# Kernel tuning notes

Measured on AMD Instinct MI355X. Metric: run time of the kernel, lower is better.

## Reference

```python
import jax, jax.numpy as jnp
import numpy as np
import math

B, S, IN_DIM = 4, 2048, 256
ATT_DIM, NUM_HEADS, TOP_K = 128, 4, 32


def _linear_params(key, out_dim, in_dim):
    kw, kb = jax.random.split(key)
    bound = 1.0 / math.sqrt(in_dim)
    w = jax.random.uniform(kw, (out_dim, in_dim), jnp.float32, -bound, bound)
    b = jax.random.uniform(kb, (out_dim,), jnp.float32, -bound, bound)
    return w, b


def setup_inputs() -> dict:
    key = jax.random.key(0)
    keys = jax.random.split(key, 16)
    x = jax.random.normal(keys[0], (B, S, IN_DIM), jnp.float32)
    tp_w, tp_b = _linear_params(keys[1], ATT_DIM, IN_DIM)
    sp_w, sp_b = _linear_params(keys[2], ATT_DIM, IN_DIM)
    ta_qw, ta_qb = _linear_params(keys[3], ATT_DIM, ATT_DIM)
    ta_kw, ta_kb = _linear_params(keys[4], ATT_DIM, ATT_DIM)
    ta_vw, ta_vb = _linear_params(keys[5], ATT_DIM, ATT_DIM)
    ta_ow, ta_ob = _linear_params(keys[6], ATT_DIM, ATT_DIM)
    sa_qw, sa_qb = _linear_params(keys[7], ATT_DIM, ATT_DIM)
    sa_kw, sa_kb = _linear_params(keys[8], ATT_DIM, ATT_DIM)
    sa_vw, sa_vb = _linear_params(keys[9], ATT_DIM, ATT_DIM)
    sa_ow, sa_ob = _linear_params(keys[10], ATT_DIM, ATT_DIM)
    gate_w, gate_b = _linear_params(keys[11], ATT_DIM, 2 * ATT_DIM)
    fus_w, fus_b = _linear_params(keys[12], ATT_DIM, 2 * ATT_DIM)
    return dict(x=x, tp_w=tp_w, tp_b=tp_b, sp_w=sp_w, sp_b=sp_b,
                ta_qw=ta_qw, ta_qb=ta_qb, ta_kw=ta_kw, ta_kb=ta_kb,
                ta_vw=ta_vw, ta_vb=ta_vb, ta_ow=ta_ow, ta_ob=ta_ob,
                sa_qw=sa_qw, sa_qb=sa_qb, sa_kw=sa_kw, sa_kb=sa_kb,
                sa_vw=sa_vw, sa_vb=sa_vb, sa_ow=sa_ow, sa_ob=sa_ob,
                gate_w=gate_w, gate_b=gate_b, fus_w=fus_w, fus_b=fus_b)


def _lin(x, w, b):
    return x @ w.T + b


def _sparse_topk_attention(x, qw, qb, kw, kb, vw, vb, ow, ob):
    # x: [B, S, E]; dropout is identity in eval mode
    b, s, e = x.shape
    h, d = NUM_HEADS, e // NUM_HEADS
    q = _lin(x, qw, qb).reshape(b, s, h, d).transpose(0, 2, 1, 3)  # [B,H,S,D]
    k = _lin(x, kw, kb).reshape(b, s, h, d).transpose(0, 2, 1, 3)
    v = _lin(x, vw, vb).reshape(b, s, h, d).transpose(0, 2, 1, 3)
    scores = jnp.einsum('bhqd,bhkd->bhqk', q, k) / math.sqrt(d)  # [B,H,S,S]
    kk = min(TOP_K, s)
    top_scores, top_idx = jax.lax.top_k(scores, kk)  # [B,H,S,K]
    soft = jax.nn.softmax(top_scores, axis=-1)
    # scatter softmaxed top-k weights into a zero [B,H,S,S] matrix (faithful to source)
    bi = jnp.arange(b)[:, None, None, None]
    hi = jnp.arange(h)[None, :, None, None]
    si = jnp.arange(s)[None, None, :, None]
    sparse = jnp.zeros_like(scores).at[bi, hi, si, top_idx].set(soft)
    out = jnp.einsum('bhqk,bhkd->bhqd', sparse, v)
    out = out.transpose(0, 2, 1, 3).reshape(b, s, e)
    return _lin(out, ow, ob)


def reference(x, tp_w, tp_b, sp_w, sp_b,
              ta_qw, ta_qb, ta_kw, ta_kb, ta_vw, ta_vb, ta_ow, ta_ob,
              sa_qw, sa_qb, sa_kw, sa_kb, sa_vw, sa_vb, sa_ow, sa_ob,
              gate_w, gate_b, fus_w, fus_b):
    temporal = _lin(x, tp_w, tp_b)
    temporal = _sparse_topk_attention(temporal, ta_qw, ta_qb, ta_kw, ta_kb,
                                      ta_vw, ta_vb, ta_ow, ta_ob)
    semantic = _lin(x, sp_w, sp_b)
    semantic = _sparse_topk_attention(semantic, sa_qw, sa_qb, sa_kw, sa_kb,
                                      sa_vw, sa_vb, sa_ow, sa_ob)
    concat = jnp.concatenate([temporal, semantic], axis=-1)  # [B,S,2A]
    gate = jax.nn.sigmoid(_lin(concat, gate_w, gate_b))
    fused = _lin(concat, fus_w, fus_b) * gate
    return fused
```

## Files before the change

### kernel.cpp

```cpp
#include <hip/hip_runtime.h>
#include <math.h>

#define B_   4
#define S_   2048
#define AD   128
#define NH   4
#define HD   32
#define TK   32
#define SEG  1048576
#define CAP  192

#define OFF_PROJ 0
#define OFF_Q    (1 * SEG)
#define OFF_K    (2 * SEG)
#define OFF_V    (3 * SEG)
#define OFF_ATT  (4 * SEG)
#define OFF_T    (5 * SEG)
#define OFF_SB   (6 * SEG)
#define OFF_CAT  (7 * SEG)

__device__ float g_ws[9 * SEG];
__device__ float g_sc[8 * S_ * S_];

__device__ __forceinline__ unsigned f2key(float s) {
    unsigned u = __float_as_uint(s);
    return (u & 0x80000000u) ? ~u : (u | 0x80000000u);
}
__device__ __forceinline__ float key2f(unsigned k) {
    unsigned u = (k & 0x80000000u) ? (k & 0x7FFFFFFFu) : ~k;
    return __uint_as_float(u);
}

template <int KD>
__global__ __launch_bounds__(256)
void lin_kernel(const float* __restrict__ Xext, int xoff,
                const float* __restrict__ W, const float* __restrict__ Bv,
                int yoff)
{
    const float* X = Xext ? Xext : (const float*)(g_ws + xoff);
    float* Y = g_ws + yoff;
    __shared__ float Xs[32][72];
    __shared__ float Ws[32][72];
    const int bm = blockIdx.x * 64;
    const int bn = blockIdx.y * 64;
    const int t  = threadIdx.x;
    const int tx = t & 15, ty = t >> 4;
    const int sr = t >> 3, sc4 = t & 7;
    float acc[4][4] = {};
    for (int kk = 0; kk < KD; kk += 32) {
        #pragma unroll
        for (int it = 0; it < 2; ++it) {
            int rr = sr + it * 32;
            float4 xa = *(const float4*)(X + (size_t)(bm + rr) * KD + kk + sc4 * 4);
            float4 wa = *(const float4*)(W + (size_t)(bn + rr) * KD + kk + sc4 * 4);
            Xs[sc4*4+0][rr] = xa.x; Xs[sc4*4+1][rr] = xa.y;
            Xs[sc4*4+2][rr] = xa.z; Xs[sc4*4+3][rr] = xa.w;
            Ws[sc4*4+0][rr] = wa.x; Ws[sc4*4+1][rr] = wa.y;
            Ws[sc4*4+2][rr] = wa.z; Ws[sc4*4+3][rr] = wa.w;
        }
        __syncthreads();
        #pragma unroll
        for (int kc = 0; kc < 32; ++kc) {
            float4 a4 = *(const float4*)&Xs[kc][ty * 4];
            float4 b4 = *(const float4*)&Ws[kc][tx * 4];
            float a[4] = {a4.x, a4.y, a4.z, a4.w};
            float bb[4] = {b4.x, b4.y, b4.z, b4.w};
            #pragma unroll
            for (int i = 0; i < 4; ++i)
                #pragma unroll
                for (int j = 0; j < 4; ++j)
                    acc[i][j] = fmaf(a[i], bb[j], acc[i][j]);
        }
        __syncthreads();
    }
    #pragma unroll
    for (int i = 0; i < 4; ++i) {
        int row = bm + ty * 4 + i;
        int col = bn + tx * 4;
        float4 o;
        o.x = acc[i][0] + Bv[col + 0]; o.y = acc[i][1] + Bv[col + 1];
        o.z = acc[i][2] + Bv[col + 2]; o.w = acc[i][3] + Bv[col + 3];
        *(float4*)(Y + (size_t)row * AD + col) = o;
    }
}

template <int KD>
__global__ __launch_bounds__(256)
void lin3_kernel(int xoff,
                 const float* __restrict__ W0, const float* __restrict__ B0, int y0,
                 const float* __restrict__ W1, const float* __restrict__ B1, int y1,
                 const float* __restrict__ W2, const float* __restrict__ B2, int y2)
{
    const int z = blockIdx.z;
    const float* X = (const float*)(g_ws + xoff);
    const float* W = (z == 0) ? W0 : (z == 1) ? W1 : W2;
    const float* Bv = (z == 0) ? B0 : (z == 1) ? B1 : B2;
    float* Y = g_ws + ((z == 0) ? y0 : (z == 1) ? y1 : y2);
    __shared__ float Xs[32][72];
    __shared__ float Ws[32][72];
    const int bm = blockIdx.x * 64;
    const int bn = blockIdx.y * 64;
    const int t  = threadIdx.x;
    const int tx = t & 15, ty = t >> 4;
    const int sr = t >> 3, sc4 = t & 7;
    float acc[4][4] = {};
    for (int kk = 0; kk < KD; kk += 32) {
        #pragma unroll
        for (int it = 0; it < 2; ++it) {
            int rr = sr + it * 32;
            float4 xa = *(const float4*)(X + (size_t)(bm + rr) * KD + kk + sc4 * 4);
            float4 wa = *(const float4*)(W + (size_t)(bn + rr) * KD + kk + sc4 * 4);
            Xs[sc4*4+0][rr] = xa.x; Xs[sc4*4+1][rr] = xa.y;
            Xs[sc4*4+2][rr] = xa.z; Xs[sc4*4+3][rr] = xa.w;
            Ws[sc4*4+0][rr] = wa.x; Ws[sc4*4+1][rr] = wa.y;
            Ws[sc4*4+2][rr] = wa.z; Ws[sc4*4+3][rr] = wa.w;
        }
        __syncthreads();
        #pragma unroll
        for (int kc = 0; kc < 32; ++kc) {
            float4 a4 = *(const float4*)&Xs[kc][ty * 4];
            float4 b4 = *(const float4*)&Ws[kc][tx * 4];
            float a[4] = {a4.x, a4.y, a4.z, a4.w};
            float bb[4] = {b4.x, b4.y, b4.z, b4.w};
            #pragma unroll
            for (int i = 0; i < 4; ++i)
                #pragma unroll
                for (int j = 0; j < 4; ++j)
                    acc[i][j] = fmaf(a[i], bb[j], acc[i][j]);
        }
        __syncthreads();
    }
    #pragma unroll
    for (int i = 0; i < 4; ++i) {
        int row = bm + ty * 4 + i;
        int col = bn + tx * 4;
        float4 o;
        o.x = acc[i][0] + Bv[col + 0]; o.y = acc[i][1] + Bv[col + 1];
        o.z = acc[i][2] + Bv[col + 2]; o.w = acc[i][3] + Bv[col + 3];
        *(float4*)(Y + (size_t)row * AD + col) = o;
    }
}

__global__ __launch_bounds__(256)
void score_kernel(int qoff, int koff, int chunk)
{
    const int zh = blockIdx.z;
    const int hh = chunk * 8 + zh, b = hh >> 2, h = hh & 3;
    const float* Qb = g_ws + qoff + (size_t)b * S_ * AD + h * HD;
    const float* Kb = g_ws + koff + (size_t)b * S_ * AD + h * HD;
    float* Sc = g_sc + (size_t)zh * S_ * S_;
    __shared__ float Qs[32][72];
    __shared__ float Ks[32][72];
    const int t = threadIdx.x, tx = t & 15, ty = t >> 4;
    const int sr = t >> 3, sc4 = t & 7;
    const int q0 = blockIdx.y * 64, k0 = blockIdx.x * 64;
    #pragma unroll
    for (int it = 0; it < 2; ++it) {
        int rr = sr + it * 32;
        float4 qa = *(const float4*)(Qb + (size_t)(q0 + rr) * AD + sc4 * 4);
        float4 ka = *(const float4*)(Kb + (size_t)(k0 + rr) * AD + sc4 * 4);
        Qs[sc4*4+0][rr] = qa.x; Qs[sc4*4+1][rr] = qa.y;
        Qs[sc4*4+2][rr] = qa.z; Qs[sc4*4+3][rr] = qa.w;
        Ks[sc4*4+0][rr] = ka.x; Ks[sc4*4+1][rr] = ka.y;
        Ks[sc4*4+2][rr] = ka.z; Ks[sc4*4+3][rr] = ka.w;
    }
    __syncthreads();
    float acc[4][4] = {};
    #pragma unroll
    for (int kc = 0; kc < 32; ++kc) {
        float4 a4 = *(const float4*)&Qs[kc][ty * 4];
        float4 b4 = *(const float4*)&Ks[kc][tx * 4];
        float a[4] = {a4.x, a4.y, a4.z, a4.w};
        float bb[4] = {b4.x, b4.y, b4.z, b4.w};
        #pragma unroll
        for (int i = 0; i < 4; ++i)
            #pragma unroll
            for (int j = 0; j < 4; ++j)
                acc[i][j] = fmaf(a[i], bb[j], acc[i][j]);
    }
    const float scale = 0.17677669529663688f;
    #pragma unroll
    for (int i = 0; i < 4; ++i) {
        float4 o;
        o.x = acc[i][0] * scale; o.y = acc[i][1] * scale;
        o.z = acc[i][2] * scale; o.w = acc[i][3] * scale;
        *(float4*)(Sc + (size_t)(q0 + ty * 4 + i) * S_ + k0 + tx * 4) = o;
    }
}

__device__ __forceinline__ void select_row(const unsigned (&keys)[32],
                                           unsigned long long* sv,
                                           float* wp, unsigned* jp,
                                           int lane, unsigned thr, float Mf)
{
    int base = 0;
    const unsigned long long lt = (1ull << lane) - 1ull;
    #pragma unroll
    for (int t = 0; t < 32; ++t) {
        bool pred = keys[t] >= thr;
        unsigned long long m = __ballot(pred);
        int slot = base + __popcll(m & lt);
        if (pred && slot < CAP) {
            unsigned jidx = (unsigned)((t >> 2) * 256 + lane * 4 + (t & 3));
            sv[slot] = ((unsigned long long)keys[t] << 32) | (unsigned)(2047 - jidx);
        }
        base += __popcll(m);
    }
    const int S = base;
    asm volatile("s_waitcnt lgkmcnt(0)" ::: "memory");

    if (S <= 64) {
        unsigned long long pi = (lane < S) ? sv[lane] : 0ull;
        int rank = 0;
        for (int jx = 0; jx < S; ++jx)
            rank += (sv[jx] > pi) ? 1 : 0;
        float e = 0.f; unsigned ji = 0;
        if (lane < S && rank < TK) {
            float val = key2f((unsigned)(pi >> 32));
            e = __expf(val - Mf);
            ji = 2047u - (unsigned)(pi & 0xFFFFFFFFull);
        }
        float esum = e;
        #pragma unroll
        for (int off = 1; off < 64; off <<= 1) esum += __shfl_xor(esum, off);
        if (lane < S && rank < TK) { wp[rank] = e / esum; jp[rank] = ji; }
    } else if (S <= CAP) {
        unsigned long long pi[3]; int rk[3]; float ee[3]; unsigned jj[3];
        float esum = 0.f;
        #pragma unroll
        for (int u = 0; u < 3; ++u) {
            int i = lane + u * 64;
            pi[u] = (i < S) ? sv[i] : 0ull;
            rk[u] = 0; ee[u] = 0.f; jj[u] = 0;
        }
        for (int jx = 0; jx < S; ++jx) {
            unsigned long long pj = sv[jx];
            #pragma unroll
            for (int u = 0; u < 3; ++u)
                rk[u] += (pj > pi[u]) ? 1 : 0;
        }
        #pragma unroll
        for (int u = 0; u < 3; ++u) {
            int i = lane + u * 64;
            if (i < S && rk[u] < TK) {
                float val = key2f((unsigned)(pi[u] >> 32));
                ee[u] = __expf(val - Mf);
                jj[u] = 2047u - (unsigned)(pi[u] & 0xFFFFFFFFull);
                esum += ee[u];
            }
        }
        #pragma unroll
        for (int off = 1; off < 64; off <<= 1) esum += __shfl_xor(esum, off);
        #pragma unroll
        for (int u = 0; u < 3; ++u) {
            int i = lane + u * 64;
            if (i < S && rk[u] < TK) { wp[rk[u]] = ee[u] / esum; jp[rk[u]] = jj[u]; }
        }
    } else {
        unsigned consumed = 0u;
        for (int i = 0; i < TK; ++i) {
            unsigned bk = 0u; unsigned gj = 0xFFFFFFFFu;
            #pragma unroll
            for (int t = 0; t < 32; ++t) {
                if (((consumed >> t) & 1u) == 0u) {
                    unsigned kk = keys[t];
                    unsigned j = (unsigned)((t >> 2) * 256 + lane * 4 + (t & 3));
                    if (kk > bk || (kk == bk && j < gj)) { bk = kk; gj = j; }
                }
            }
            #pragma unroll
            for (int off = 1; off < 64; off <<= 1) {
                unsigned ok = (unsigned)__shfl_xor((int)bk, off);
                unsigned oj = (unsigned)__shfl_xor((int)gj, off);
                if (ok > bk || (ok == bk && oj < gj)) { bk = ok; gj = oj; }
            }
            if (((gj >> 2) & 63u) == (unsigned)lane && gj != 0xFFFFFFFFu) {
                int t = ((int)gj >> 8) * 4 + ((int)gj & 3);
                consumed |= (1u << t);
            }
            if (lane == 0) { wp[i] = key2f(bk); jp[i] = gj; }
        }
        asm volatile("s_waitcnt lgkmcnt(0)" ::: "memory");
        float v = (lane < TK) ? wp[lane] : 0.f;
        float e = (lane < TK) ? __expf(v - Mf) : 0.f;
        float esum = e;
        #pragma unroll
        for (int off = 1; off < 64; off <<= 1) esum += __shfl_xor(esum, off);
        if (lane < TK) wp[lane] = e / esum;
    }
    asm volatile("s_waitcnt lgkmcnt(0)" ::: "memory");
}

__global__ __launch_bounds__(256)
void topk_kernel(int voff, int ooff, int chunk)
{
    const float* V = g_ws + voff;
    float* O = g_ws + ooff;

    __shared__ unsigned long long sve[4][2][CAP];
    __shared__ float    wsel[4][2][32];
    __shared__ unsigned jsel[4][2][32];

    const int wid  = threadIdx.x >> 6;
    const int lane = threadIdx.x & 63;
    const int gr   = blockIdx.x * 4 + wid;
    const int row0 = gr * 2;
    const int zh   = row0 >> 11;
    const int q0   = row0 & 2047, q1 = q0 + 1;
    const int hh   = chunk * 8 + zh;
    const int b    = hh >> 2,  h = hh & 3;

    const float* Srow0 = g_sc + (size_t)zh * S_ * S_ + (size_t)q0 * S_;
    const float* Srow1 = Srow0 + S_;
    const float* vbase = V + (size_t)b * S_ * AD + h * HD;

    unsigned keys0[32], keys1[32];
    unsigned lmax0 = 0u, lmax1 = 0u;
    #pragma unroll
    for (int i = 0; i < 8; ++i) {
        float4 s4 = ((const float4*)Srow0)[i * 64 + lane];
        unsigned k0 = f2key(s4.x), k1 = f2key(s4.y);
        unsigned k2 = f2key(s4.z), k3 = f2key(s4.w);
        keys0[i*4+0] = k0; keys0[i*4+1] = k1; keys0[i*4+2] = k2; keys0[i*4+3] = k3;
        unsigned m01 = (k0 > k1) ? k0 : k1, m23 = (k2 > k3) ? k2 : k3;
        unsigned m = (m01 > m23) ? m01 : m23;
        lmax0 = (m > lmax0) ? m : lmax0;
    }
    #pragma unroll
    for (int i = 0; i < 8; ++i) {
        float4 s4 = ((const float4*)Srow1)[i * 64 + lane];
        unsigned k0 = f2key(s4.x), k1 = f2key(s4.y);
        unsigned k2 = f2key(s4.z), k3 = f2key(s4.w);
        keys1[i*4+0] = k0; keys1[i*4+1] = k1; keys1[i*4+2] = k2; keys1[i*4+3] = k3;
        unsigned m01 = (k0 > k1) ? k0 : k1, m23 = (k2 > k3) ? k2 : k3;
        unsigned m = (m01 > m23) ? m01 : m23;
        lmax1 = (m > lmax1) ? m : lmax1;
    }

    unsigned bs0 = lmax0, bs1 = lmax1;
    #pragma unroll
    for (int k = 2; k <= 64; k <<= 1) {
        #pragma unroll
        for (int j = k >> 1; j > 0; j >>= 1) {
            unsigned o0 = (unsigned)__shfl_xor((int)bs0, j);
            unsigned o1 = (unsigned)__shfl_xor((int)bs1, j);
            bool keepmin = (((lane & k) == 0) == ((lane & j) == 0));
            bs0 = keepmin ? (bs0 < o0 ? bs0 : o0) : (bs0 > o0 ? bs0 : o0);
            bs1 = keepmin ? (bs1 < o1 ? bs1 : o1) : (bs1 > o1 ? bs1 : o1);
        }
    }
    const unsigned thr0 = (unsigned)__shfl((int)bs0, 32);
    const unsigned thr1 = (unsigned)__shfl((int)bs1, 32);
    const float Mf0 = key2f((unsigned)__shfl((int)bs0, 63));
    const float Mf1 = key2f((unsigned)__shfl((int)bs1, 63));

    select_row(keys0, sve[wid][0], wsel[wid][0], jsel[wid][0], lane, thr0, Mf0);
    select_row(keys1, sve[wid][1], wsel[wid][1], jsel[wid][1], lane, thr1, Mf1);

    const int dd = lane & 31, half = lane >> 5;
    const float*    wp = wsel[wid][half];
    const unsigned* jp = jsel[wid][half];
    float oacc = 0.f;
    #pragma unroll
    for (int i = 0; i < 32; ++i)
        oacc = fmaf(wp[i], vbase[(size_t)jp[i] * AD + dd], oacc);
    const int qq = half ? q1 : q0;
    O[((size_t)b * S_ + qq) * AD + h * HD + dd] = oacc;
}

__global__ __launch_bounds__(256)
void concat_kernel()
{
    int i = blockIdx.x * 256 + threadIdx.x;
    int row = i >> 8, c = i & 255;
    float v = (c < AD) ? g_ws[OFF_T + row * AD + c]
                       : g_ws[OFF_SB + row * AD + (c - AD)];
    g_ws[OFF_CAT + i] = v;
}

__global__ __launch_bounds__(256)
void fuse_kernel(float* __restrict__ out)
{
    int i = blockIdx.x * 256 + threadIdx.x;
    float g = g_ws[OFF_Q + i];
    float f = g_ws[OFF_K + i];
    out[i] = f / (1.0f + expf(-g));
}

extern "C" void kernel_launch(void* const* d_in, const int* in_sizes, int n_in,
                              void* d_out, int out_size, void* d_ws, size_t ws_size,
                              hipStream_t stream)
{
    (void)in_sizes; (void)n_in; (void)d_ws; (void)ws_size; (void)out_size;
    const float* x      = (const float*)d_in[0];
    const float* tp_w   = (const float*)d_in[1];
    const float* tp_b   = (const float*)d_in[2];
    const float* sp_w   = (const float*)d_in[3];
    const float* sp_b   = (const float*)d_in[4];
    const float* gate_w = (const float*)d_in[21];
    const float* gate_b = (const float*)d_in[22];
    const float* fus_w  = (const float*)d_in[23];
    const float* fus_b  = (const float*)d_in[24];

    dim3 gl(128, 2);
    for (int br = 0; br < 2; ++br) {
        const float* pw = br ? sp_w : tp_w;
        const float* pb = br ? sp_b : tp_b;
        int base = 5 + br * 8;
        const float* qw = (const float*)d_in[base + 0];
        const float* qb = (const float*)d_in[base + 1];
        const float* kw = (const float*)d_in[base + 2];
        const float* kb = (const float*)d_in[base + 3];
        const float* vw = (const float*)d_in[base + 4];
        const float* vb = (const float*)d_in[base + 5];
        const float* ow = (const float*)d_in[base + 6];
        const float* ob = (const float*)d_in[base + 7];

        lin_kernel<256><<<gl, 256, 0, stream>>>(x, 0, pw, pb, OFF_PROJ);
        lin3_kernel<128><<<dim3(128, 2, 3), 256, 0, stream>>>(
            OFF_PROJ, qw, qb, OFF_Q, kw, kb, OFF_K, vw, vb, OFF_V);
        for (int chunk = 0; chunk < 2; ++chunk) {
            score_kernel<<<dim3(32, 32, 8), 256, 0, stream>>>(OFF_Q, OFF_K, chunk);
            topk_kernel<<<2048, 256, 0, stream>>>(OFF_V, OFF_ATT, chunk);
        }
        lin_kernel<128><<<gl, 256, 0, stream>>>(nullptr, OFF_ATT, ow, ob,
                                                br ? OFF_SB : OFF_T);
    }
    concat_kernel<<<8192, 256, 0, stream>>>();
    lin3_kernel<256><<<dim3(128, 2, 2), 256, 0, stream>>>(
        OFF_CAT, gate_w, gate_b, OFF_Q, fus_w, fus_b, OFF_K,
        (const float*)nullptr, (const float*)nullptr, 0);
    fuse_kernel<<<4096, 256, 0, stream>>>((float*)d_out);
}
```

Measured before the change: 429.0 us.

## Fuse score computation with top-k selection, removing the materialized score matrix

Replaces the separate score GEMM kernel, which wrote full SxS score matrices to global memory, with a fused kernel. The fused kernel computes dot products against double-buffered, XOR-swizzled K tiles in shared memory, keeps scores in registers, then runs top-k selection and the V gather in place. This removes the large global write and read of scores and the chunked launches. In exchange it gives up the GEMM-style register tiling for per-lane dot products with the Q row held in uniform registers. It also shrinks the LDS padding in the linear kernels.

```diff
diff --git a/kernel.cpp b/kernel.cpp
--- a/kernel.cpp
+++ b/kernel.cpp
@@ -20,7 +20,6 @@
 #define OFF_CAT  (7 * SEG)
 
 __device__ float g_ws[9 * SEG];
-__device__ float g_sc[8 * S_ * S_];
 
 __device__ __forceinline__ unsigned f2key(float s) {
     unsigned u = __float_as_uint(s);
@@ -29,6 +28,9 @@
 __device__ __forceinline__ float key2f(unsigned k) {
     unsigned u = (k & 0x80000000u) ? (k & 0x7FFFFFFFu) : ~k;
     return __uint_as_float(u);
+}
+__device__ __forceinline__ float rfl(float x) {
+    return __uint_as_float(__builtin_amdgcn_readfirstlane(__float_as_uint(x)));
 }
 
 template <int KD>
@@ -39,8 +41,8 @@
 {
     const float* X = Xext ? Xext : (const float*)(g_ws + xoff);
     float* Y = g_ws + yoff;
-    __shared__ float Xs[32][72];
-    __shared__ float Ws[32][72];
+    __shared__ float Xs[32][68];
+    __shared__ float Ws[32][68];
     const int bm = blockIdx.x * 64;
     const int bn = blockIdx.y * 64;
     const int t  = threadIdx.x;
@@ -96,8 +98,8 @@
     const float* W = (z == 0) ? W0 : (z == 1) ? W1 : W2;
     const float* Bv = (z == 0) ? B0 : (z == 1) ? B1 : B2;
     float* Y = g_ws + ((z == 0) ? y0 : (z == 1) ? y1 : y2);
-    __shared__ float Xs[32][72];
-    __shared__ float Ws[32][72];
+    __shared__ float Xs[32][68];
+    __shared__ float Ws[32][68];
     const int bm = blockIdx.x * 64;
     const int bn = blockIdx.y * 64;
     const int t  = threadIdx.x;
@@ -141,58 +143,12 @@
     }
 }
 
-__global__ __launch_bounds__(256)
-void score_kernel(int qoff, int koff, int chunk)
-{
-    const int zh = blockIdx.z;
-    const int hh = chunk * 8 + zh, b = hh >> 2, h = hh & 3;
-    const float* Qb = g_ws + qoff + (size_t)b * S_ * AD + h * HD;
-    const float* Kb = g_ws + koff + (size_t)b * S_ * AD + h * HD;
-    float* Sc = g_sc + (size_t)zh * S_ * S_;
-    __shared__ float Qs[32][72];
-    __shared__ float Ks[32][72];
-    const int t = threadIdx.x, tx = t & 15, ty = t >> 4;
-    const int sr = t >> 3, sc4 = t & 7;
-    const int q0 = blockIdx.y * 64, k0 = blockIdx.x * 64;
-    #pragma unroll
-    for (int it = 0; it < 2; ++it) {
-        int rr = sr + it * 32;
-        float4 qa = *(const float4*)(Qb + (size_t)(q0 + rr) * AD + sc4 * 4);
-        float4 ka = *(const float4*)(Kb + (size_t)(k0 + rr) * AD + sc4 * 4);
-        Qs[sc4*4+0][rr] = qa.x; Qs[sc4*4+1][rr] = qa.y;
-        Qs[sc4*4+2][rr] = qa.z; Qs[sc4*4+3][rr] = qa.w;
-        Ks[sc4*4+0][rr] = ka.x; Ks[sc4*4+1][rr] = ka.y;
-        Ks[sc4*4+2][rr] = ka.z; Ks[sc4*4+3][rr] = ka.w;
-    }
-    __syncthreads();
-    float acc[4][4] = {};
-    #pragma unroll
-    for (int kc = 0; kc < 32; ++kc) {
-        float4 a4 = *(const float4*)&Qs[kc][ty * 4];
-        float4 b4 = *(const float4*)&Ks[kc][tx * 4];
-        float a[4] = {a4.x, a4.y, a4.z, a4.w};
-        float bb[4] = {b4.x, b4.y, b4.z, b4.w};
-        #pragma unroll
-        for (int i = 0; i < 4; ++i)
-            #pragma unroll
-            for (int j = 0; j < 4; ++j)
-                acc[i][j] = fmaf(a[i], bb[j], acc[i][j]);
-    }
-    const float scale = 0.17677669529663688f;
-    #pragma unroll
-    for (int i = 0; i < 4; ++i) {
-        float4 o;
-        o.x = acc[i][0] * scale; o.y = acc[i][1] * scale;
-        o.z = acc[i][2] * scale; o.w = acc[i][3] * scale;
-        *(float4*)(Sc + (size_t)(q0 + ty * 4 + i) * S_ + k0 + tx * 4) = o;
-    }
-}
-
 __device__ __forceinline__ void select_row(const unsigned (&keys)[32],
                                            unsigned long long* sv,
                                            float* wp, unsigned* jp,
                                            int lane, unsigned thr, float Mf)
 {
+    asm volatile("s_waitcnt lgkmcnt(0)" ::: "memory");
     int base = 0;
     const unsigned long long lt = (1ull << lane) - 1ull;
     #pragma unroll
@@ -201,7 +157,7 @@
         unsigned long long m = __ballot(pred);
         int slot = base + __popcll(m & lt);
         if (pred && slot < CAP) {
-            unsigned jidx = (unsigned)((t >> 2) * 256 + lane * 4 + (t & 3));
+            unsigned jidx = (unsigned)(t * 64 + lane);
             sv[slot] = ((unsigned long long)keys[t] << 32) | (unsigned)(2047 - jidx);
         }
         base += __popcll(m);
@@ -264,7 +220,7 @@
             for (int t = 0; t < 32; ++t) {
                 if (((consumed >> t) & 1u) == 0u) {
                     unsigned kk = keys[t];
-                    unsigned j = (unsigned)((t >> 2) * 256 + lane * 4 + (t & 3));
+                    unsigned j = (unsigned)(t * 64 + lane);
                     if (kk > bk || (kk == bk && j < gj)) { bk = kk; gj = j; }
                 }
             }
@@ -274,10 +230,8 @@
                 unsigned oj = (unsigned)__shfl_xor((int)gj, off);
                 if (ok > bk || (ok == bk && oj < gj)) { bk = ok; gj = oj; }
             }
-            if (((gj >> 2) & 63u) == (unsigned)lane && gj != 0xFFFFFFFFu) {
-                int t = ((int)gj >> 8) * 4 + ((int)gj & 3);
-                consumed |= (1u << t);
-            }
+            if ((gj & 63u) == (unsigned)lane && gj != 0xFFFFFFFFu)
+                consumed |= (1u << (gj >> 6));
             if (lane == 0) { wp[i] = key2f(bk); jp[i] = gj; }
         }
         asm volatile("s_waitcnt lgkmcnt(0)" ::: "memory");
@@ -292,49 +246,79 @@
 }
 
 __global__ __launch_bounds__(256)
-void topk_kernel(int voff, int ooff, int chunk)
-{
-    const float* V = g_ws + voff;
+void fused_attn(int qoff, int koff, int voff, int ooff)
+{
+    __shared__ float4 Ks[2][64][8];
+    __shared__ unsigned long long sve[4][CAP];
+    __shared__ float    wsel[4][32];
+    __shared__ unsigned jsel[4][32];
+
+    const int tid  = threadIdx.x;
+    const int wid  = tid >> 6;
+    const int lane = tid & 63;
+    const int hh   = blockIdx.y;
+    const int b    = hh >> 2, h = hh & 3;
+    const int r0   = blockIdx.x * 8 + wid * 2;
+
+    const float* Qb    = g_ws + qoff + (size_t)b * S_ * AD + h * HD;
+    const float* Kb    = g_ws + koff + (size_t)b * S_ * AD + h * HD;
+    const float* vbase = g_ws + voff + (size_t)b * S_ * AD + h * HD;
     float* O = g_ws + ooff;
 
-    __shared__ unsigned long long sve[4][2][CAP];
-    __shared__ float    wsel[4][2][32];
-    __shared__ unsigned jsel[4][2][32];
-
-    const int wid  = threadIdx.x >> 6;
-    const int lane = threadIdx.x & 63;
-    const int gr   = blockIdx.x * 4 + wid;
-    const int row0 = gr * 2;
-    const int zh   = row0 >> 11;
-    const int q0   = row0 & 2047, q1 = q0 + 1;
-    const int hh   = chunk * 8 + zh;
-    const int b    = hh >> 2,  h = hh & 3;
-
-    const float* Srow0 = g_sc + (size_t)zh * S_ * S_ + (size_t)q0 * S_;
-    const float* Srow1 = Srow0 + S_;
-    const float* vbase = V + (size_t)b * S_ * AD + h * HD;
+    const float scale = 0.17677669529663688f;
+
+    float qs0[32], qs1[32];
+    #pragma unroll
+    for (int g = 0; g < 8; ++g) {
+        float4 qa = *(const float4*)(Qb + (size_t)r0 * AD + g * 4);
+        float4 qb = *(const float4*)(Qb + (size_t)(r0 + 1) * AD + g * 4);
+        qs0[g*4+0] = rfl(qa.x) * scale; qs0[g*4+1] = rfl(qa.y) * scale;
+        qs0[g*4+2] = rfl(qa.z) * scale; qs0[g*4+3] = rfl(qa.w) * scale;
+        qs1[g*4+0] = rfl(qb.x) * scale; qs1[g*4+1] = rfl(qb.y) * scale;
+        qs1[g*4+2] = rfl(qb.z) * scale; qs1[g*4+3] = rfl(qb.w) * scale;
+    }
+
+    const int srow = tid >> 2;
+    const int sgp  = (tid & 3) * 2;
+    const int sg0  = sgp ^ (srow & 7);
+    const int sg1  = (sgp + 1) ^ (srow & 7);
+    const size_t sbase = (size_t)srow * AD + sgp * 4;
+
+    {
+        float4 a = *(const float4*)(Kb + sbase);
+        float4 c = *(const float4*)(Kb + sbase + 4);
+        Ks[0][srow][sg0] = a;
+        Ks[0][srow][sg1] = c;
+    }
+    __syncthreads();
 
     unsigned keys0[32], keys1[32];
     unsigned lmax0 = 0u, lmax1 = 0u;
-    #pragma unroll
-    for (int i = 0; i < 8; ++i) {
-        float4 s4 = ((const float4*)Srow0)[i * 64 + lane];
-        unsigned k0 = f2key(s4.x), k1 = f2key(s4.y);
-        unsigned k2 = f2key(s4.z), k3 = f2key(s4.w);
-        keys0[i*4+0] = k0; keys0[i*4+1] = k1; keys0[i*4+2] = k2; keys0[i*4+3] = k3;
-        unsigned m01 = (k0 > k1) ? k0 : k1, m23 = (k2 > k3) ? k2 : k3;
-        unsigned m = (m01 > m23) ? m01 : m23;
-        lmax0 = (m > lmax0) ? m : lmax0;
-    }
-    #pragma unroll
-    for (int i = 0; i < 8; ++i) {
-        float4 s4 = ((const float4*)Srow1)[i * 64 + lane];
-        unsigned k0 = f2key(s4.x), k1 = f2key(s4.y);
-        unsigned k2 = f2key(s4.z), k3 = f2key(s4.w);
-        keys1[i*4+0] = k0; keys1[i*4+1] = k1; keys1[i*4+2] = k2; keys1[i*4+3] = k3;
-        unsigned m01 = (k0 > k1) ? k0 : k1, m23 = (k2 > k3) ? k2 : k3;
-        unsigned m = (m01 > m23) ? m01 : m23;
-        lmax1 = (m > lmax1) ? m : lmax1;
+    const int l7 = lane & 7;
+
+    #pragma unroll
+    for (int t = 0; t < 32; ++t) {
+        const int cur = t & 1;
+        if (t < 31) {
+            float4 a = *(const float4*)(Kb + (size_t)(t + 1) * 64 * AD + sbase);
+            float4 c = *(const float4*)(Kb + (size_t)(t + 1) * 64 * AD + sbase + 4);
+            Ks[cur ^ 1][srow][sg0] = a;
+            Ks[cur ^ 1][srow][sg1] = c;
+        }
+        float s0 = 0.f, s1 = 0.f;
+        #pragma unroll
+        for (int g = 0; g < 8; ++g) {
+            float4 kv = Ks[cur][lane][g ^ l7];
+            s0 = fmaf(qs0[g*4+0], kv.x, s0); s0 = fmaf(qs0[g*4+1], kv.y, s0);
+            s0 = fmaf(qs0[g*4+2], kv.z, s0); s0 = fmaf(qs0[g*4+3], kv.w, s0);
+            s1 = fmaf(qs1[g*4+0], kv.x, s1); s1 = fmaf(qs1[g*4+1], kv.y, s1);
+            s1 = fmaf(qs1[g*4+2], kv.z, s1); s1 = fmaf(qs1[g*4+3], kv.w, s1);
+        }
+        unsigned k0 = f2key(s0), k1 = f2key(s1);
+        keys0[t] = k0; keys1[t] = k1;
+        lmax0 = (k0 > lmax0) ? k0 : lmax0;
+        lmax1 = (k1 > lmax1) ? k1 : lmax1;
+        __syncthreads();
     }
 
     unsigned bs0 = lmax0, bs1 = lmax1;
@@ -354,18 +338,30 @@
     const float Mf0 = key2f((unsigned)__shfl((int)bs0, 63));
     const float Mf1 = key2f((unsigned)__shfl((int)bs1, 63));
 
-    select_row(keys0, sve[wid][0], wsel[wid][0], jsel[wid][0], lane, thr0, Mf0);
-    select_row(keys1, sve[wid][1], wsel[wid][1], jsel[wid][1], lane, thr1, Mf1);
-
     const int dd = lane & 31, half = lane >> 5;
-    const float*    wp = wsel[wid][half];
-    const unsigned* jp = jsel[wid][half];
-    float oacc = 0.f;
-    #pragma unroll
-    for (int i = 0; i < 32; ++i)
-        oacc = fmaf(wp[i], vbase[(size_t)jp[i] * AD + dd], oacc);
-    const int qq = half ? q1 : q0;
-    O[((size_t)b * S_ + qq) * AD + h * HD + dd] = oacc;
+
+    select_row(keys0, sve[wid], wsel[wid], jsel[wid], lane, thr0, Mf0);
+    {
+        float oacc = 0.f;
+        #pragma unroll
+        for (int u = 0; u < 16; ++u) {
+            int i = half * 16 + u;
+            oacc = fmaf(wsel[wid][i], vbase[(size_t)jsel[wid][i] * AD + dd], oacc);
+        }
+        oacc += __shfl_down(oacc, 32);
+        if (lane < HD) O[((size_t)b * S_ + r0) * AD + h * HD + lane] = oacc;
+    }
+    select_row(keys1, sve[wid], wsel[wid], jsel[wid], lane, thr1, Mf1);
+    {
+        float oacc = 0.f;
+        #pragma unroll
+        for (int u = 0; u < 16; ++u) {
+            int i = half * 16 + u;
+            oacc = fmaf(wsel[wid][i], vbase[(size_t)jsel[wid][i] * AD + dd], oacc);
+        }
+        oacc += __shfl_down(oacc, 32);
+        if (lane < HD) O[((size_t)b * S_ + r0 + 1) * AD + h * HD + lane] = oacc;
+    }
 }
 
 __global__ __launch_bounds__(256)
@@ -419,10 +415,7 @@
         lin_kernel<256><<<gl, 256, 0, stream>>>(x, 0, pw, pb, OFF_PROJ);
         lin3_kernel<128><<<dim3(128, 2, 3), 256, 0, stream>>>(
             OFF_PROJ, qw, qb, OFF_Q, kw, kb, OFF_K, vw, vb, OFF_V);
-        for (int chunk = 0; chunk < 2; ++chunk) {
-            score_kernel<<<dim3(32, 32, 8), 256, 0, stream>>>(OFF_Q, OFF_K, chunk);
-            topk_kernel<<<2048, 256, 0, stream>>>(OFF_V, OFF_ATT, chunk);
-        }
+        fused_attn<<<dim3(256, 16), 256, 0, stream>>>(OFF_Q, OFF_K, OFF_V, OFF_ATT);
         lin_kernel<128><<<gl, 256, 0, stream>>>(nullptr, OFF_ATT, ow, ob,
                                                 br ? OFF_SB : OFF_T);
     }
```

Result: slower. 793.2 us (+84.9%).
